# Optimization experiments

Measured on AMD Instinct MI355X. Metric: run time of the kernel, lower is better.

Reference implementation:

```python
import jax, jax.numpy as jnp
import numpy as np

IN_F, HID, OUT = 768, 64, 1
BATCH = 131072
NNZ1 = int(0.1 * IN_F * HID)   # 4915
NNZ2 = int(0.1 * HID * HID)    # 409
NNZ3 = int(0.5 * HID * OUT)    # 32


def _coo(key, nnz, n_rows, n_cols):
    kr, kc, kv = jax.random.split(key, 3)
    rows = jax.random.randint(kr, (nnz,), 0, n_rows, dtype=jnp.int32)
    cols = jax.random.randint(kc, (nnz,), 0, n_cols, dtype=jnp.int32)
    vals = jax.random.normal(kv, (nnz,), dtype=jnp.float32)
    return jnp.stack([rows, cols]), vals


def setup_inputs() -> dict:
    key = jax.random.key(0)
    kx, k1, k2, k3, kb1, kb2, kb3 = jax.random.split(key, 7)
    x = jax.random.normal(kx, (BATCH, IN_F), dtype=jnp.float32)
    idx1, val1 = _coo(k1, NNZ1, IN_F, HID)
    idx2, val2 = _coo(k2, NNZ2, HID, HID)
    idx3, val3 = _coo(k3, NNZ3, HID, OUT)
    b1 = jax.random.normal(kb1, (HID,), dtype=jnp.float32)
    b2 = jax.random.normal(kb2, (HID,), dtype=jnp.float32)
    b3 = jax.random.normal(kb3, (OUT,), dtype=jnp.float32)
    return {"x": x, "idx1": idx1, "val1": val1, "b1": b1,
            "idx2": idx2, "val2": val2, "b2": b2,
            "idx3": idx3, "val3": val3, "b3": b3}


def _densify(idx, vals, shape):
    # COO -> dense; duplicate indices accumulate (torch coalesce semantics)
    return jnp.zeros(shape, dtype=vals.dtype).at[idx[0], idx[1]].add(vals)


def reference(x, idx1, val1, b1, idx2, val2, b2, idx3, val3, b3):
    x = x.reshape(x.shape[0], -1)                      # [B, IN_F]
    W1 = _densify(idx1, val1, (IN_F, HID))
    W2 = _densify(idx2, val2, (HID, HID))
    W3 = _densify(idx3, val3, (HID, OUT))
    h = jax.nn.relu(x @ W1 + b1)                       # [B, 64]
    h = jax.nn.relu(h @ W2 + b2)                       # [B, 64]
    return h @ W3 + b3                                 # [B, 1]
```

## Files before the change

### kernel.cpp

```cpp
#include <hip/hip_runtime.h>
#include <cstdint>
#include <cstddef>

#define IN_F 768
#define HID  64
#define NNZ1 4915
#define NNZ2 409
#define NNZ3 32
#define BATCH 131072

#define OFF_W1D 0u
#define OFF_W2D 196608u
#define OFF_W3D 212992u
#define OFF_W1F 213248u
#define OFF_W2F 311552u
#define WS_NEED 319744u

typedef __bf16 bf16x8 __attribute__((ext_vector_type(8)));
typedef float  f32x4  __attribute__((ext_vector_type(4)));
typedef float  f32x8  __attribute__((ext_vector_type(8)));

union FragU { bf16x8 v; uint32_t u[4]; uint4 q; };
union F8U   { float4 f4[2]; f32x8 v8; };

__device__ __forceinline__ uint32_t f2bf1(float f) {
    uint32_t u = __float_as_uint(f);
    return (u + 0x7FFFu + ((u >> 16) & 1u)) >> 16;
}
__device__ __forceinline__ uint32_t f2bf2(float lo, float hi) {
    uint32_t a = __float_as_uint(lo);
    uint32_t b = __float_as_uint(hi);
    a = a + 0x7FFFu + ((a >> 16) & 1u);
    b = b + 0x7FFFu + ((b >> 16) & 1u);
    return (a >> 16) | (b & 0xFFFF0000u);
}

__device__ __forceinline__ bf16x8 pack8(float4 a, float4 b) {
    F8U u; u.f4[0] = a; u.f4[1] = b;
    return __builtin_convertvector(u.v8, bf16x8);
}

__global__ void scatter_coo(const int* __restrict__ idx1, const float* __restrict__ val1,
                            const int* __restrict__ idx2, const float* __restrict__ val2,
                            const int* __restrict__ idx3, const float* __restrict__ val3,
                            float* __restrict__ W1d, float* __restrict__ W2d,
                            float* __restrict__ W3d) {
    int t = blockIdx.x * blockDim.x + threadIdx.x;
    if (t < NNZ1) {
        int r = idx1[t], c = idx1[NNZ1 + t];
        atomicAdd(&W1d[r * HID + c], val1[t]);
    } else if (t < NNZ1 + NNZ2) {
        int i = t - NNZ1;
        int r = idx2[i], c = idx2[NNZ2 + i];
        atomicAdd(&W2d[r * HID + c], val2[i]);
    } else if (t < NNZ1 + NNZ2 + NNZ3) {
        int i = t - NNZ1 - NNZ2;
        int r = idx3[i], c = idx3[NNZ3 + i];
        atomicAdd(&W3d[r * 1 + c], val3[i]);
    }
}

__global__ void frag_build(const float* __restrict__ W1d, const float* __restrict__ W2d,
                           uint4* __restrict__ W1f, uint4* __restrict__ W2f) {
    int t = blockIdx.x * blockDim.x + threadIdx.x;
    const int n1 = 24 * 4 * 64;
    const int n2 = 2 * 4 * 64;
    if (t < n1) {
        int lane = t & 63;
        int fi = t >> 6;
        int kstep = fi >> 2, nt = fi & 3;
        int m = lane & 15, quad = lane >> 4;
        int kbase = (kstep >> 1) * 64 + quad * 16 + (kstep & 1) * 8;
        uint32_t u[4];
#pragma unroll
        for (int jj = 0; jj < 4; ++jj) {
            int k = kbase + jj * 2;
            u[jj] = f2bf2(W1d[k * HID + nt * 16 + m], W1d[(k + 1) * HID + nt * 16 + m]);
        }
        W1f[t] = make_uint4(u[0], u[1], u[2], u[3]);
    } else if (t < n1 + n2) {
        int tt = t - n1;
        int lane = tt & 63;
        int fi = tt >> 6;
        int kstep = fi >> 2, nt = fi & 3;
        int m = lane & 15, quad = lane >> 4;
        uint32_t u[4];
#pragma unroll
        for (int jj = 0; jj < 4; ++jj) {
            int k = kstep * 32 + quad * 8 + jj * 2;
            u[jj] = f2bf2(W2d[k * HID + nt * 16 + m], W2d[(k + 1) * HID + nt * 16 + m]);
        }
        W2f[tt] = make_uint4(u[0], u[1], u[2], u[3]);
    }
}

template<int CB>
__device__ __forceinline__ void window_body(
    int win,
    const float* __restrict__ xr, const uint4* __restrict__ w1p,
    float4 (&xw)[2][4], uint4 (&bqC)[8], uint4 (&bqN)[8], f32x4 (&acc)[4])
{
    if (win + 1 < 12) {
        const uint4* bp = w1p + (size_t)(win + 1) * 8 * 64;
#pragma unroll
        for (int i = 0; i < 8; ++i) bqN[i] = bp[i * 64];
    }
    const float4 x0 = xw[CB][0], x1 = xw[CB][1], x2 = xw[CB][2], x3 = xw[CB][3];
    if (win < 10) {
#pragma unroll
        for (int i = 0; i < 4; ++i)
            xw[CB][i] = *(const float4*)(xr + (win + 2) * 64 + i * 4);
    }
    FragU a0, a1;
    a0.v = pack8(x0, x1);
    a1.v = pack8(x2, x3);
#pragma unroll
    for (int nt = 0; nt < 4; ++nt) {
        FragU bb; bb.q = bqC[nt];
        acc[nt] = __builtin_amdgcn_mfma_f32_16x16x32_bf16(a0.v, bb.v, acc[nt], 0, 0, 0);
    }
#pragma unroll
    for (int nt = 0; nt < 4; ++nt) {
        FragU bb; bb.q = bqC[4 + nt];
        acc[nt] = __builtin_amdgcn_mfma_f32_16x16x32_bf16(a1.v, bb.v, acc[nt], 0, 0, 0);
    }
}

__global__ __launch_bounds__(256) void mlp_fused(
    const float* __restrict__ x,
    const uint4* __restrict__ W1f,
    const uint4* __restrict__ W2f,
    const float* __restrict__ W3d,
    const float* __restrict__ b1,
    const float* __restrict__ b2,
    const float* __restrict__ b3,
    float* __restrict__ out)
{
    __shared__ __align__(16) uint16_t h1s[4][16][72];

    const int lane = threadIdx.x & 63;
    const int w    = threadIdx.x >> 6;
    const int m    = lane & 15;
    const int quad = lane >> 4;
    const int rowbase = blockIdx.x * 64 + w * 16;

    f32x4 acc[4] = {{0,0,0,0},{0,0,0,0},{0,0,0,0},{0,0,0,0}};

    const float* xr = x + (size_t)(rowbase + m) * IN_F + quad * 16;
    const uint4* w1p = W1f + lane;

    uint4 bqA[8], bqB[8];
#pragma unroll
    for (int i = 0; i < 8; ++i) bqA[i] = w1p[i * 64];

    float4 xw[2][4];
#pragma unroll
    for (int i = 0; i < 4; ++i) {
        xw[0][i] = *(const float4*)(xr + 0 * 64 + i * 4);
        xw[1][i] = *(const float4*)(xr + 1 * 64 + i * 4);
    }

#pragma unroll 1
    for (int wp = 0; wp < 6; ++wp) {
        window_body<0>(2 * wp,     xr, w1p, xw, bqA, bqB, acc);
        window_body<1>(2 * wp + 1, xr, w1p, xw, bqB, bqA, acc);
    }

#pragma unroll
    for (int nt = 0; nt < 4; ++nt) {
        const int col = nt * 16 + m;
        const float bias = b1[col];
#pragma unroll
        for (int r = 0; r < 4; ++r) {
            float h = acc[nt][r] + bias;
            h = h > 0.f ? h : 0.f;
            h1s[w][quad * 4 + r][col] = (uint16_t)f2bf1(h);
        }
    }

    f32x4 acc2[4] = {{0,0,0,0},{0,0,0,0},{0,0,0,0},{0,0,0,0}};
#pragma unroll
    for (int k2 = 0; k2 < 2; ++k2) {
        FragU a2;
        a2.q = *(const uint4*)&h1s[w][m][k2 * 32 + quad * 8];
#pragma unroll
        for (int nt = 0; nt < 4; ++nt) {
            FragU bb; bb.q = W2f[(k2 * 4 + nt) * 64 + lane];
            acc2[nt] = __builtin_amdgcn_mfma_f32_16x16x32_bf16(a2.v, bb.v, acc2[nt], 0, 0, 0);
        }
    }

    float w3v[4];
#pragma unroll
    for (int nt = 0; nt < 4; ++nt) w3v[nt] = W3d[nt * 16 + m];

    float p[4] = {0.f, 0.f, 0.f, 0.f};
#pragma unroll
    for (int nt = 0; nt < 4; ++nt) {
        const float bias = b2[nt * 16 + m];
#pragma unroll
        for (int r = 0; r < 4; ++r) {
            float h = acc2[nt][r] + bias;
            h = h > 0.f ? h : 0.f;
            p[r] += h * w3v[nt];
        }
    }
#pragma unroll
    for (int off = 1; off < 16; off <<= 1) {
#pragma unroll
        for (int r = 0; r < 4; ++r) p[r] += __shfl_xor(p[r], off, 16);
    }
    const float bb3 = b3[0];
    if (m == 0) {
#pragma unroll
        for (int r = 0; r < 4; ++r) out[rowbase + quad * 4 + r] = p[r] + bb3;
    }
}

extern "C" void kernel_launch(void* const* d_in, const int* in_sizes, int n_in,
                              void* d_out, int out_size, void* d_ws, size_t ws_size,
                              hipStream_t stream) {
    const float* x    = (const float*)d_in[0];
    const int*   idx1 = (const int*)  d_in[1];
    const float* val1 = (const float*)d_in[2];
    const float* b1   = (const float*)d_in[3];
    const int*   idx2 = (const int*)  d_in[4];
    const float* val2 = (const float*)d_in[5];
    const float* b2   = (const float*)d_in[6];
    const int*   idx3 = (const int*)  d_in[7];
    const float* val3 = (const float*)d_in[8];
    const float* b3   = (const float*)d_in[9];
    float* out = (float*)d_out;

    char* ws = (char*)d_ws;
    float* W1d = (float*)(ws + OFF_W1D);
    float* W2d = (float*)(ws + OFF_W2D);
    float* W3d = (float*)(ws + OFF_W3D);
    uint4* W1f = (uint4*)(ws + OFF_W1F);
    uint4* W2f = (uint4*)(ws + OFF_W2F);

    hipMemsetAsync(d_ws, 0, OFF_W1F, stream);

    const int nnz_total = NNZ1 + NNZ2 + NNZ3;
    scatter_coo<<<(nnz_total + 255) / 256, 256, 0, stream>>>(
        idx1, val1, idx2, val2, idx3, val3, W1d, W2d, W3d);

    const int nfrag = 24 * 4 * 64 + 2 * 4 * 64;
    frag_build<<<(nfrag + 255) / 256, 256, 0, stream>>>(W1d, W2d, W1f, W2f);

    mlp_fused<<<BATCH / 64, 256, 0, stream>>>(x, W1f, W2f, W3d, b1, b2, b3, out);
}
```

Baseline: 555.1 us.

## Split layer-1 K reduction across wave pairs with LDS partial-sum combine

Each 16-row tile is now computed by two waves, each covering half of the 768-wide input dimension; the second wave writes its partial accumulators to shared memory and the first adds them before the bias/ReLU and later layers. Blocks cover 32 rows instead of 64, doubling the grid. The intent is to shorten the serial per-wave load/MFMA chain and expose more concurrent memory requests for the streaming x reads, at the cost of an extra LDS round trip, a block barrier, and half the waves idling in the epilogue.

```diff
diff --git a/kernel.cpp b/kernel.cpp
--- a/kernel.cpp
+++ b/kernel.cpp
@@ -96,20 +96,20 @@
 
 template<int CB>
 __device__ __forceinline__ void window_body(
-    int win,
+    int lw,
     const float* __restrict__ xr, const uint4* __restrict__ w1p,
     float4 (&xw)[2][4], uint4 (&bqC)[8], uint4 (&bqN)[8], f32x4 (&acc)[4])
 {
-    if (win + 1 < 12) {
-        const uint4* bp = w1p + (size_t)(win + 1) * 8 * 64;
+    if (lw + 1 < 6) {
+        const uint4* bp = w1p + (size_t)(lw + 1) * 8 * 64;
 #pragma unroll
         for (int i = 0; i < 8; ++i) bqN[i] = bp[i * 64];
     }
     const float4 x0 = xw[CB][0], x1 = xw[CB][1], x2 = xw[CB][2], x3 = xw[CB][3];
-    if (win < 10) {
+    if (lw < 4) {
 #pragma unroll
         for (int i = 0; i < 4; ++i)
-            xw[CB][i] = *(const float4*)(xr + (win + 2) * 64 + i * 4);
+            xw[CB][i] = *(const float4*)(xr + (lw + 2) * 64 + i * 4);
     }
     FragU a0, a1;
     a0.v = pack8(x0, x1);
@@ -136,18 +136,21 @@
     const float* __restrict__ b3,
     float* __restrict__ out)
 {
-    __shared__ __align__(16) uint16_t h1s[4][16][72];
+    __shared__ __align__(16) uint16_t h1s[2][16][72];
+    __shared__ __align__(16) f32x4 pacc[2][4][64];
 
     const int lane = threadIdx.x & 63;
     const int w    = threadIdx.x >> 6;
+    const int p    = w >> 1;
+    const int h    = w & 1;
     const int m    = lane & 15;
     const int quad = lane >> 4;
-    const int rowbase = blockIdx.x * 64 + w * 16;
+    const int rowbase = blockIdx.x * 32 + p * 16;
 
     f32x4 acc[4] = {{0,0,0,0},{0,0,0,0},{0,0,0,0},{0,0,0,0}};
 
-    const float* xr = x + (size_t)(rowbase + m) * IN_F + quad * 16;
-    const uint4* w1p = W1f + lane;
+    const float* xr = x + (size_t)(rowbase + m) * IN_F + quad * 16 + h * 384;
+    const uint4* w1p = W1f + (size_t)h * 6 * 8 * 64 + lane;
 
     uint4 bqA[8], bqB[8];
 #pragma unroll
@@ -161,20 +164,29 @@
     }
 
 #pragma unroll 1
-    for (int wp = 0; wp < 6; ++wp) {
+    for (int wp = 0; wp < 3; ++wp) {
         window_body<0>(2 * wp,     xr, w1p, xw, bqA, bqB, acc);
         window_body<1>(2 * wp + 1, xr, w1p, xw, bqB, bqA, acc);
     }
 
+    if (h == 1) {
+#pragma unroll
+        for (int nt = 0; nt < 4; ++nt) pacc[p][nt][lane] = acc[nt];
+    }
+    __syncthreads();
+    if (h == 1) return;
+#pragma unroll
+    for (int nt = 0; nt < 4; ++nt) acc[nt] += pacc[p][nt][lane];
+
 #pragma unroll
     for (int nt = 0; nt < 4; ++nt) {
         const int col = nt * 16 + m;
         const float bias = b1[col];
 #pragma unroll
         for (int r = 0; r < 4; ++r) {
-            float h = acc[nt][r] + bias;
-            h = h > 0.f ? h : 0.f;
-            h1s[w][quad * 4 + r][col] = (uint16_t)f2bf1(h);
+            float hv = acc[nt][r] + bias;
+            hv = hv > 0.f ? hv : 0.f;
+            h1s[p][quad * 4 + r][col] = (uint16_t)f2bf1(hv);
         }
     }
 
@@ -182,7 +194,7 @@
 #pragma unroll
     for (int k2 = 0; k2 < 2; ++k2) {
         FragU a2;
-        a2.q = *(const uint4*)&h1s[w][m][k2 * 32 + quad * 8];
+        a2.q = *(const uint4*)&h1s[p][m][k2 * 32 + quad * 8];
 #pragma unroll
         for (int nt = 0; nt < 4; ++nt) {
             FragU bb; bb.q = W2f[(k2 * 4 + nt) * 64 + lane];
@@ -194,26 +206,26 @@
 #pragma unroll
     for (int nt = 0; nt < 4; ++nt) w3v[nt] = W3d[nt * 16 + m];
 
-    float p[4] = {0.f, 0.f, 0.f, 0.f};
+    float pr[4] = {0.f, 0.f, 0.f, 0.f};
 #pragma unroll
     for (int nt = 0; nt < 4; ++nt) {
         const float bias = b2[nt * 16 + m];
 #pragma unroll
         for (int r = 0; r < 4; ++r) {
-            float h = acc2[nt][r] + bias;
-            h = h > 0.f ? h : 0.f;
-            p[r] += h * w3v[nt];
+            float hv = acc2[nt][r] + bias;
+            hv = hv > 0.f ? hv : 0.f;
+            pr[r] += hv * w3v[nt];
         }
     }
 #pragma unroll
     for (int off = 1; off < 16; off <<= 1) {
 #pragma unroll
-        for (int r = 0; r < 4; ++r) p[r] += __shfl_xor(p[r], off, 16);
+        for (int r = 0; r < 4; ++r) pr[r] += __shfl_xor(pr[r], off, 16);
     }
     const float bb3 = b3[0];
     if (m == 0) {
 #pragma unroll
-        for (int r = 0; r < 4; ++r) out[rowbase + quad * 4 + r] = p[r] + bb3;
+        for (int r = 0; r < 4; ++r) out[rowbase + quad * 4 + r] = pr[r] + bb3;
     }
 }
 
@@ -248,5 +260,5 @@
     const int nfrag = 24 * 4 * 64 + 2 * 4 * 64;
     frag_build<<<(nfrag + 255) / 256, 256, 0, stream>>>(W1d, W2d, W1f, W2f);
 
-    mlp_fused<<<BATCH / 64, 256, 0, stream>>>(x, W1f, W2f, W3d, b1, b2, b3, out);
-}
+    mlp_fused<<<BATCH / 32, 256, 0, stream>>>(x, W1f, W2f, W3d, b1, b2, b3, out);
+}
```

Result: no change. 549.3 us (-1.0%).
